# Kernel optimization log

Measured on AMD Instinct MI355X. Metric: run time of the kernel, lower is better.

Reference implementation:

```python
import jax, jax.numpy as jnp
import numpy as np

B, T, DIM, HEADS, MLP_H, R = 64, 197, 768, 12, 3072, 16
HD = DIM // HEADS
EPS = 1e-5
R_EFF = min(R, (T - 1) // 2)  # class token protected


def layernorm(x, g, b):
    m = jnp.mean(x, -1, keepdims=True)
    v = jnp.var(x, -1, keepdims=True)
    return (x - m) * jax.lax.rsqrt(v + EPS) * g + b


def matching_indices(metric):
    # metric: [B, T, HD]; class token (index 0 of 'a' set) protected
    metric = metric / jnp.linalg.norm(metric, axis=-1, keepdims=True)
    a, b = metric[:, ::2], metric[:, 1::2]            # [B,ta,d], [B,tb,d]
    scores = jnp.einsum('bic,bjc->bij', a, b)
    scores = scores.at[:, 0, :].set(-jnp.inf)         # protect cls token
    node_max = jnp.max(scores, axis=-1)
    node_idx = jnp.argmax(scores, axis=-1)
    edge_idx = jnp.argsort(-node_max, axis=-1)        # descending similarity
    unm_idx = edge_idx[:, R_EFF:]
    src_idx = edge_idx[:, :R_EFF]
    dst_idx = jnp.take_along_axis(node_idx, src_idx, axis=-1)
    unm_idx = jnp.sort(unm_idx, axis=1)               # keep cls first (cls token)
    return unm_idx, src_idx, dst_idx


def merge(x, unm_idx, src_idx, dst_idx):
    # x: [B, T, c] -> [B, T - R_EFF, c]; always scatter-add (as in source code)
    src, dst = x[:, ::2], x[:, 1::2]
    unm = jnp.take_along_axis(src, unm_idx[..., None], axis=1)
    sel = jnp.take_along_axis(src, src_idx[..., None], axis=1)
    bidx = jnp.arange(x.shape[0])[:, None]
    dst = dst.at[bidx, dst_idx].add(sel)
    return jnp.concatenate([unm, dst], axis=1)


def block(x, attn_size, ln1_g, ln1_b, w_qkv, w_proj, b_proj,
          ln2_g, ln2_b, w_fc1, b_fc1, w_fc2, b_fc2):
    # --- attention with log-size bias ---
    h = layernorm(x, ln1_g, ln1_b)
    qkv = (h @ w_qkv.T).reshape(B, T, 3, HEADS, HD).transpose(2, 0, 3, 1, 4)
    q, k, v = qkv[0], qkv[1], qkv[2]                  # [B,H,T,HD]
    attn = jnp.einsum('bhid,bhjd->bhij', q, k) * (HD ** -0.5)
    attn = attn + jnp.log(attn_size)[:, None, None, :, 0]
    attn = jax.nn.softmax(attn, axis=-1)
    o = jnp.einsum('bhij,bhjd->bhid', attn, v).transpose(0, 2, 1, 3).reshape(B, T, DIM)
    x = x + (o @ w_proj.T + b_proj)
    metric = jax.lax.stop_gradient(jnp.mean(k, axis=1))  # [B,T,HD]; no_grad in torch
    # --- ToMe bipartite soft matching ---
    unm_idx, src_idx, dst_idx = matching_indices(metric)
    # source tracking (adjacency initial tokens -> merged groups)
    source = jnp.broadcast_to(jnp.eye(T, dtype=x.dtype), (B, T, T))
    source = merge(source, unm_idx, src_idx, dst_idx)     # [B, Tn, T]
    tn = source.shape[1]
    rci = jnp.max(source * jnp.arange(1, tn + 1, dtype=x.dtype)[:, None], axis=-2)
    rci = (rci - 2.0)[:, 1:]                              # cls_token branch
    # size-weighted average merge
    xs = merge(x * attn_size, unm_idx, src_idx, dst_idx)
    new_size = merge(attn_size, unm_idx, src_idx, dst_idx)
    x = xs / new_size
    # --- MLP ---
    h2 = layernorm(x, ln2_g, ln2_b)
    h2 = jax.nn.gelu(h2 @ w_fc1.T + b_fc1, approximate=False)
    x = x + (h2 @ w_fc2.T + b_fc2)
    return x, new_size, rci


def setup_inputs() -> dict:
    key = jax.random.key(0)
    ks = jax.random.split(key, 6)
    return dict(
        x=jax.random.normal(ks[0], (B, T, DIM), jnp.float32),
        attn_size=jnp.ones((B, T, 1), jnp.float32),
        ln1_g=jnp.ones((DIM,), jnp.float32),
        ln1_b=jnp.zeros((DIM,), jnp.float32),
        w_qkv=jax.random.normal(ks[1], (3 * DIM, DIM), jnp.float32) * 0.02,
        w_proj=jax.random.normal(ks[2], (DIM, DIM), jnp.float32) * 0.02,
        b_proj=jnp.zeros((DIM,), jnp.float32),
        ln2_g=jnp.ones((DIM,), jnp.float32),
        ln2_b=jnp.zeros((DIM,), jnp.float32),
        w_fc1=jax.random.normal(ks[3], (MLP_H, DIM), jnp.float32) * 0.02,
        b_fc1=jnp.zeros((MLP_H,), jnp.float32),
        w_fc2=jax.random.normal(ks[4], (DIM, MLP_H), jnp.float32) * 0.02,
        b_fc2=jnp.zeros((DIM,), jnp.float32),
    )


def reference(x, attn_size, ln1_g, ln1_b, w_qkv, w_proj, b_proj,
              ln2_g, ln2_b, w_fc1, b_fc1, w_fc2, b_fc2):
    return block(x, attn_size, ln1_g, ln1_b, w_qkv, w_proj, b_proj,
                 ln2_g, ln2_b, w_fc1, b_fc1, w_fc2, b_fc2)
```

## Files before the change

### kernel.cpp

```cpp
#include <hip/hip_runtime.h>
#include <cstdint>
#include <cstddef>

#define DEVFN __device__ __forceinline__

typedef __attribute__((ext_vector_type(8))) short short8;
typedef __attribute__((ext_vector_type(4))) float f32x4;
typedef __attribute__((ext_vector_type(2))) long long2v;

#define GLOAD_LDS16(gaddr, laddr)                                              \
  __builtin_amdgcn_global_load_lds(                                            \
      (const __attribute__((address_space(1))) uint32_t*)(gaddr),              \
      (__attribute__((address_space(3))) uint32_t*)(laddr), 16, 0, 0)

constexpr int B_ = 64, T_ = 197, DIM_ = 768, H_ = 12, HD_ = 64, MLP_ = 3072;
constexpr int N_ = B_ * T_;
constexpr int NE_ = 99, NO_ = 98, REFF_ = 16;
constexpr int TM_ = (NE_ - REFF_) + NO_;
constexpr int NM_ = B_ * TM_;

constexpr size_t BOFF_A    = 0;
constexpr size_t BOFF_GBC  = 0;
constexpr size_t BOFF_B    = 58097664;
constexpr size_t BOFF_C    = 77463552;
constexpr size_t BOFF_D    = 113049600;
constexpr size_t BOFF_WKM  = 130842624;
constexpr size_t BOFF_RT   = 131039232;
constexpr size_t BOFF_NSZ  = 131873280;
constexpr size_t BOFF_WQB  = 131919616;
constexpr size_t BOFF_WPB  = 135458560;
constexpr size_t BOFF_W1B  = 136638208;
constexpr size_t BOFF_W2B  = 141356800;

DEVFN ushort f2b(float f) {
  union { float f; uint u; } c; c.f = f;
  uint u = c.u;
  u = (u + 0x7FFFu + ((u >> 16) & 1u)) >> 16;
  return (ushort)u;
}
DEVFN float b2f(ushort h) {
  union { uint u; float f; } c; c.u = ((uint)h) << 16;
  return c.f;
}
DEVFN uchar f2e4m3(float v) {
  return (uchar)__builtin_amdgcn_cvt_pk_fp8_f32(v, 0.f, 0, false);
}
DEVFN uint pk4_fp8(float a, float b, float c, float d) {
  int r = __builtin_amdgcn_cvt_pk_fp8_f32(a, b, 0, false);
  r = __builtin_amdgcn_cvt_pk_fp8_f32(c, d, r, true);
  return (uint)r;
}

DEVFN float fast_gelu(float x) {
  float x3 = x * x * x;
  float z2 = 2.0f * 0.7978845608028654f * fmaf(0.044715f, x3, x);
  z2 = fminf(fmaxf(z2, -60.0f), 60.0f);
  float e = __expf(z2);
  float th = (e - 1.0f) / (e + 1.0f);
  return 0.5f * x * (1.0f + th);
}

DEVFN float wave_sum(float v) {
#pragma unroll
  for (int o = 32; o; o >>= 1) v += __shfl_down(v, o, 64);
  return v;
}
DEVFN float block_sum(float v, float* red) {
  v = wave_sum(v);
  int lane = threadIdx.x & 63, wid = threadIdx.x >> 6;
  __syncthreads();
  if (lane == 0) red[wid] = v;
  __syncthreads();
  return red[0] + red[1] + red[2] + red[3];
}

constexpr int SEG0 = 3 * DIM_ * DIM_;
constexpr int SEG1 = SEG0 + DIM_ * DIM_;
constexpr int SEG2 = SEG1 + MLP_ * DIM_;
constexpr int SEG3 = SEG2 + DIM_ * MLP_;
__global__ __launch_bounds__(256) void f2ball_kernel(
    const float* __restrict__ s0, const float* __restrict__ s1,
    const float* __restrict__ s2, const float* __restrict__ s3,
    uchar* __restrict__ d0, ushort* __restrict__ d1,
    uchar* __restrict__ d2, uchar* __restrict__ d3) {
  int i = (blockIdx.x * 256 + threadIdx.x) * 4;
  if (i >= SEG3) return;
  if (i >= SEG0 && i < SEG1) {
    int off = i - SEG0;
    float4 v = *reinterpret_cast<const float4*>(s1 + off);
    ushort4 o;
    o.x = f2b(v.x); o.y = f2b(v.y); o.z = f2b(v.z); o.w = f2b(v.w);
    *reinterpret_cast<ushort4*>(d1 + off) = o;
  } else {
    const float* src; uchar* dst; int off;
    if (i < SEG0)      { src = s0; dst = d0; off = i; }
    else if (i < SEG2) { src = s2; dst = d2; off = i - SEG1; }
    else               { src = s3; dst = d3; off = i - SEG2; }
    float4 v = *reinterpret_cast<const float4*>(src + off);
    *reinterpret_cast<uint*>(dst + off) = pk4_fp8(v.x, v.y, v.z, v.w);
  }
}

__global__ __launch_bounds__(256) void ln_kernel(
    const float* __restrict__ x, const float* __restrict__ g,
    const float* __restrict__ bb, float* __restrict__ outf,
    uchar* __restrict__ out8) {
  __shared__ float red[4];
  size_t row = blockIdx.x;
  const float* xr = x + row * DIM_;
  int tid = threadIdx.x;
  float s = 0.f;
  for (int i = tid; i < DIM_; i += 256) s += xr[i];
  s = block_sum(s, red);
  float mean = s * (1.0f / DIM_);
  float vs = 0.f;
  for (int i = tid; i < DIM_; i += 256) { float d = xr[i] - mean; vs = fmaf(d, d, vs); }
  vs = block_sum(vs, red);
  float rstd = rsqrtf(vs * (1.0f / DIM_) + 1e-5f);
  for (int i = tid; i < DIM_; i += 256) {
    float v = (xr[i] - mean) * rstd * g[i] + bb[i];
    if (outf) outf[row * DIM_ + i] = v;
    out8[row * DIM_ + i] = f2e4m3(v);
  }
}

__global__ __launch_bounds__(256) void wkmean_kernel(const float* __restrict__ wqkv,
                                                     float* __restrict__ wkm) {
  int idx = blockIdx.x * 256 + threadIdx.x;
  if (idx >= HD_ * DIM_) return;
  int d = idx / DIM_, c = idx % DIM_;
  float s = 0.f;
  for (int h2 = 0; h2 < H_; h2++) s += wqkv[(size_t)(DIM_ + h2 * HD_ + d) * DIM_ + c];
  wkm[idx] = s * (1.0f / H_);
}

__global__ __launch_bounds__(256) void gemm_bt(
    const float* __restrict__ A, const float* __restrict__ Bm,
    float* __restrict__ C, int M, int Nn, int K) {
  __shared__ float As[16][65];
  __shared__ float Bs[16][65];
  const int tid = threadIdx.x;
  const int tx = tid & 15, ty = tid >> 4;
  const int m0 = blockIdx.y * 64, n0 = blockIdx.x * 64;
  float acc[4][4] = {};
  for (int k0 = 0; k0 < K; k0 += 16) {
#pragma unroll
    for (int l = 0; l < 4; ++l) {
      int idx = tid + l * 256;
      int mm = idx >> 4, kk = idx & 15;
      As[kk][mm] = A[(size_t)(m0 + mm) * K + (k0 + kk)];
      Bs[kk][mm] = Bm[(size_t)(n0 + mm) * K + (k0 + kk)];
    }
    __syncthreads();
#pragma unroll
    for (int kk = 0; kk < 16; ++kk) {
      float av[4], bv[4];
#pragma unroll
      for (int i = 0; i < 4; i++) av[i] = As[kk][ty * 4 + i];
#pragma unroll
      for (int j = 0; j < 4; j++) bv[j] = Bs[kk][tx * 4 + j];
#pragma unroll
      for (int i = 0; i < 4; i++)
#pragma unroll
        for (int j = 0; j < 4; j++) acc[i][j] = fmaf(av[i], bv[j], acc[i][j]);
    }
    __syncthreads();
  }
#pragma unroll
  for (int i = 0; i < 4; i++) {
    size_t base = (size_t)(m0 + ty * 4 + i) * Nn + n0 + tx * 4;
#pragma unroll
    for (int j = 0; j < 4; j++) C[base + j] = acc[i][j];
  }
}

__global__ __launch_bounds__(256) void gemm_mfma(
    const ushort* __restrict__ A, const ushort* __restrict__ Bw,
    const float* __restrict__ bias, const float* __restrict__ res,
    float* __restrict__ Cf, ushort* __restrict__ Cb,
    int M, int Nn, int K, int act) {
  __shared__ ushort As[3][128][32];
  __shared__ ushort Bs[3][128][32];
  const int t = threadIdx.x;
  const int wid = t >> 6, l = t & 63;
  const int wrow = wid >> 1, wcol = wid & 1;
  const int lr = l & 15, lk = l >> 4;
  const int lrow = l >> 2, lseg = l & 3;
  const int sswz = lseg ^ ((lrow >> 1) & 3);
  const int rswz = (lr >> 1) & 3;

  const int nwg = (int)gridDim.x;
  const int gx = Nn >> 7;
  const int bid = (int)blockIdx.x;
  const int q = nwg >> 3, r = nwg & 7;
  const int xcd = bid & 7, sub = bid >> 3;
  const int wgid = (xcd < r ? xcd * (q + 1) : r * (q + 1) + (xcd - r) * q) + sub;
  const int m0 = (wgid / gx) * 128, n0 = (wgid % gx) * 128;

  int rA0 = m0 + wid * 32 + lrow;      rA0 = rA0 < M ? rA0 : M - 1;
  int rA1 = m0 + wid * 32 + 16 + lrow; rA1 = rA1 < M ? rA1 : M - 1;
  const ushort* gA0 = A + (size_t)rA0 * K + sswz * 8;
  const ushort* gA1 = A + (size_t)rA1 * K + sswz * 8;
  const ushort* gB0 = Bw + (size_t)(n0 + wid * 32 + lrow) * K + sswz * 8;
  const ushort* gB1 = Bw + (size_t)(n0 + wid * 32 + 16 + lrow) * K + sswz * 8;

  f32x4 acc[4][4];
#pragma unroll
  for (int i = 0; i < 4; i++)
#pragma unroll
    for (int j = 0; j < 4; j++) acc[i][j] = (f32x4){0.f, 0.f, 0.f, 0.f};

  auto STAGE = [&](int buf, int kt) {
    const int k0 = kt * 32;
    GLOAD_LDS16(gA0 + k0, &As[buf][wid * 32][0]);
    GLOAD_LDS16(gB0 + k0, &Bs[buf][wid * 32][0]);
    GLOAD_LDS16(gA1 + k0, &As[buf][wid * 32 + 16][0]);
    GLOAD_LDS16(gB1 + k0, &Bs[buf][wid * 32 + 16][0]);
  };

  const int NT = K >> 5;
  STAGE(0, 0);
  STAGE(1, 1);
  asm volatile("s_waitcnt vmcnt(4)" ::: "memory");
  __builtin_amdgcn_s_barrier();

  for (int kt = 0; kt < NT; kt++) {
    const bool ahead = (kt + 2 < NT);
    if (ahead) STAGE((kt + 2) % 3, kt + 2);
    const int cur = kt % 3;
    short8 af[4], bf[4];
#pragma unroll
    for (int mi = 0; mi < 4; mi++)
      af[mi] = *reinterpret_cast<const short8*>(
          &As[cur][wrow * 64 + mi * 16 + lr][(lk ^ rswz) * 8]);
#pragma unroll
    for (int nj = 0; nj < 4; nj++)
      bf[nj] = *reinterpret_cast<const short8*>(
          &Bs[cur][wcol * 64 + nj * 16 + lr][(lk ^ rswz) * 8]);
#pragma unroll
    for (int mi = 0; mi < 4; mi++)
#pragma unroll
      for (int nj = 0; nj < 4; nj++)
        acc[mi][nj] = __builtin_amdgcn_mfma_f32_16x16x32_bf16(af[mi], bf[nj], acc[mi][nj], 0, 0, 0);
    if (ahead) asm volatile("s_waitcnt vmcnt(4)" ::: "memory");
    else       asm volatile("s_waitcnt vmcnt(0)" ::: "memory");
    __builtin_amdgcn_s_barrier();
  }

#pragma unroll
  for (int mi = 0; mi < 4; mi++) {
    int rbase = m0 + wrow * 64 + mi * 16 + lk * 4;
#pragma unroll
    for (int nj = 0; nj < 4; nj++) {
      int col = n0 + wcol * 64 + nj * 16 + lr;
      float bv = bias ? bias[col] : 0.f;
#pragma unroll
      for (int j = 0; j < 4; j++) {
        int row = rbase + j;
        if (row >= M) continue;
        float v = acc[mi][nj][j] + bv;
        if (act) v = fast_gelu(v);
        size_t idx = (size_t)row * Nn + col;
        if (res) v += res[idx];
        if (Cf) Cf[idx] = v;
        else Cb[idx] = f2b(v);
      }
    }
  }
}

__global__ __launch_bounds__(512) void gemm_fp8_w(
    const uchar* __restrict__ A, const uchar* __restrict__ Bw,
    const float* __restrict__ bias, ushort* __restrict__ Cb,
    uchar* __restrict__ C8, int M, int Nn, int K, int act) {
  __shared__ uchar As[3][128][64];
  __shared__ uchar Bs[3][256][64];
  const int t = threadIdx.x;
  const int wid = t >> 6, l = t & 63;
  const int wm = wid >> 2, wn = wid & 3;
  const int lr = l & 15, lk = l >> 4;
  const int l4 = l >> 2, lseg = l & 3;
  const int sswz = lseg ^ ((l4 >> 1) & 3);
  const int roff = (lk ^ ((lr >> 1) & 3)) * 16;

  const int nwg = (int)gridDim.x;
  const int gx = Nn >> 8;
  const int bid = (int)blockIdx.x;
  const int q = nwg >> 3, r = nwg & 7;
  const int xcd = bid & 7, sub = bid >> 3;
  const int wgid = (xcd < r ? xcd * (q + 1) : r * (q + 1) + (xcd - r) * q) + sub;
  const int m0 = (wgid / gx) * 128, n0 = (wgid % gx) * 256;

  int rA = m0 + wid * 16 + l4; rA = rA < M ? rA : M - 1;
  const uchar* gA0 = A + (size_t)rA * K + sswz * 16;
  const uchar* gB0 = Bw + (size_t)(n0 + wid * 32 + l4) * K + sswz * 16;
  const uchar* gB1 = Bw + (size_t)(n0 + wid * 32 + 16 + l4) * K + sswz * 16;

  f32x4 acc[4][4];
#pragma unroll
  for (int i = 0; i < 4; i++)
#pragma unroll
    for (int j = 0; j < 4; j++) acc[i][j] = (f32x4){0.f, 0.f, 0.f, 0.f};

  auto STAGE = [&](int buf, int kt) {
    const int k0 = kt * 64;
    GLOAD_LDS16(gA0 + k0, &As[buf][wid * 16][0]);
    GLOAD_LDS16(gB0 + k0, &Bs[buf][wid * 32][0]);
    GLOAD_LDS16(gB1 + k0, &Bs[buf][wid * 32 + 16][0]);
  };

  const int NT = K >> 6;
  STAGE(0, 0);
  STAGE(1, 1);
  asm volatile("s_waitcnt vmcnt(3)" ::: "memory");
  __builtin_amdgcn_s_barrier();

  for (int kt = 0; kt < NT; kt++) {
    const bool ahead = (kt + 2 < NT);
    if (ahead) STAGE((kt + 2) % 3, kt + 2);
    const int cur = kt % 3;
    long2v av[4], bv[4];
#pragma unroll
    for (int mi = 0; mi < 4; mi++)
      av[mi] = *reinterpret_cast<const long2v*>(&As[cur][wm * 64 + mi * 16 + lr][roff]);
#pragma unroll
    for (int nj = 0; nj < 4; nj++)
      bv[nj] = *reinterpret_cast<const long2v*>(&Bs[cur][wn * 64 + nj * 16 + lr][roff]);
#pragma unroll
    for (int mi = 0; mi < 4; mi++)
#pragma unroll
      for (int nj = 0; nj < 4; nj++)
        acc[mi][nj] = __builtin_amdgcn_mfma_f32_16x16x32_fp8_fp8(
            av[mi].x, bv[nj].x, acc[mi][nj], 0, 0, 0);
#pragma unroll
    for (int mi = 0; mi < 4; mi++)
#pragma unroll
      for (int nj = 0; nj < 4; nj++)
        acc[mi][nj] = __builtin_amdgcn_mfma_f32_16x16x32_fp8_fp8(
            av[mi].y, bv[nj].y, acc[mi][nj], 0, 0, 0);
    if (ahead) asm volatile("s_waitcnt vmcnt(3)" ::: "memory");
    else       asm volatile("s_waitcnt vmcnt(0)" ::: "memory");
    __builtin_amdgcn_s_barrier();
  }

#pragma unroll
  for (int mi = 0; mi < 4; mi++) {
    int rbase = m0 + wm * 64 + mi * 16 + lk * 4;
#pragma unroll
    for (int nj = 0; nj < 4; nj++) {
      int col = n0 + wn * 64 + nj * 16 + lr;
      float bvv = bias ? bias[col] : 0.f;
#pragma unroll
      for (int j = 0; j < 4; j++) {
        int row = rbase + j;
        if (row >= M) continue;
        float v = acc[mi][nj][j] + bvv;
        if (act) v = fast_gelu(v);
        size_t idx = (size_t)row * Nn + col;
        if (Cb) Cb[idx] = f2b(v);
        else C8[idx] = f2e4m3(v);
      }
    }
  }
}

__global__ __launch_bounds__(256) void gemm_fp8(
    const uchar* __restrict__ A, const uchar* __restrict__ Bw,
    const float* __restrict__ bias, const float* __restrict__ res,
    float* __restrict__ Cf, int M, int Nn, int K) {
  __shared__ uchar As[3][128][64];
  __shared__ uchar Bs[3][128][64];
  const int t = threadIdx.x;
  const int wid = t >> 6, l = t & 63;
  const int wrow = wid >> 1, wcol = wid & 1;
  const int lr = l & 15, lk = l >> 4;
  const int l4 = l >> 2, lseg = l & 3;
  const int sswz = lseg ^ ((l4 >> 1) & 3);
  const int roff = (lk ^ ((lr >> 1) & 3)) * 16;

  const int nwg = (int)gridDim.x;
  const int gx = Nn >> 7;
  const int bid = (int)blockIdx.x;
  const int q = nwg >> 3, r = nwg & 7;
  const int xcd = bid & 7, sub = bid >> 3;
  const int wgid = (xcd < r ? xcd * (q + 1) : r * (q + 1) + (xcd - r) * q) + sub;
  const int m0 = (wgid / gx) * 128, n0 = (wgid % gx) * 128;

  int rA0 = m0 + wid * 32 + l4;      rA0 = rA0 < M ? rA0 : M - 1;
  int rA1 = m0 + wid * 32 + 16 + l4; rA1 = rA1 < M ? rA1 : M - 1;
  const uchar* gA0 = A + (size_t)rA0 * K + sswz * 16;
  const uchar* gA1 = A + (size_t)rA1 * K + sswz * 16;
  const uchar* gB0 = Bw + (size_t)(n0 + wid * 32 + l4) * K + sswz * 16;
  const uchar* gB1 = Bw + (size_t)(n0 + wid * 32 + 16 + l4) * K + sswz * 16;

  f32x4 acc[4][4];
#pragma unroll
  for (int i = 0; i < 4; i++)
#pragma unroll
    for (int j = 0; j < 4; j++) acc[i][j] = (f32x4){0.f, 0.f, 0.f, 0.f};

  auto STAGE = [&](int buf, int kt) {
    const int k0 = kt * 64;
    GLOAD_LDS16(gA0 + k0, &As[buf][wid * 32][0]);
    GLOAD_LDS16(gB0 + k0, &Bs[buf][wid * 32][0]);
    GLOAD_LDS16(gA1 + k0, &As[buf][wid * 32 + 16][0]);
    GLOAD_LDS16(gB1 + k0, &Bs[buf][wid * 32 + 16][0]);
  };

  const int NT = K >> 6;
  STAGE(0, 0);
  STAGE(1, 1);
  asm volatile("s_waitcnt vmcnt(4)" ::: "memory");
  __builtin_amdgcn_s_barrier();

  for (int kt = 0; kt < NT; kt++) {
    const bool ahead = (kt + 2 < NT);
    if (ahead) STAGE((kt + 2) % 3, kt + 2);
    const int cur = kt % 3;
    long2v av[4], bv[4];
#pragma unroll
    for (int mi = 0; mi < 4; mi++)
      av[mi] = *reinterpret_cast<const long2v*>(&As[cur][wrow * 64 + mi * 16 + lr][roff]);
#pragma unroll
    for (int nj = 0; nj < 4; nj++)
      bv[nj] = *reinterpret_cast<const long2v*>(&Bs[cur][wcol * 64 + nj * 16 + lr][roff]);
#pragma unroll
    for (int mi = 0; mi < 4; mi++)
#pragma unroll
      for (int nj = 0; nj < 4; nj++)
        acc[mi][nj] = __builtin_amdgcn_mfma_f32_16x16x32_fp8_fp8(
            av[mi].x, bv[nj].x, acc[mi][nj], 0, 0, 0);
#pragma unroll
    for (int mi = 0; mi < 4; mi++)
#pragma unroll
      for (int nj = 0; nj < 4; nj++)
        acc[mi][nj] = __builtin_amdgcn_mfma_f32_16x16x32_fp8_fp8(
            av[mi].y, bv[nj].y, acc[mi][nj], 0, 0, 0);
    if (ahead) asm volatile("s_waitcnt vmcnt(4)" ::: "memory");
    else       asm volatile("s_waitcnt vmcnt(0)" ::: "memory");
    __builtin_amdgcn_s_barrier();
  }

#pragma unroll
  for (int mi = 0; mi < 4; mi++) {
    int rbase = m0 + wrow * 64 + mi * 16 + lk * 4;
#pragma unroll
    for (int nj = 0; nj < 4; nj++) {
      int col = n0 + wcol * 64 + nj * 16 + lr;
      float bvv = bias[col];
#pragma unroll
      for (int j = 0; j < 4; j++) {
        int row = rbase + j;
        if (row >= M) continue;
        size_t idx = (size_t)row * Nn + col;
        Cf[idx] = acc[mi][nj][j] + bvv + res[idx];
      }
    }
  }
}

__global__ __launch_bounds__(512) void attn3_kernel(
    const ushort* __restrict__ qkv, const float* __restrict__ asize,
    ushort* __restrict__ o) {
  __shared__ ushort Kb[208][72];
  __shared__ ushort Vt[64][232];
  __shared__ ushort Plds[8][16][232];
  __shared__ float lb[200];
  const int bh = blockIdx.x;
  const int h = bh % H_, b = bh / H_;
  const size_t bT = (size_t)b * T_;
  const int tid = threadIdx.x;
  const int l = tid & 63, wid = tid >> 6;
  const int lr = l & 15, lk = l >> 4;

  for (int j = tid; j < T_; j += 512) lb[j] = logf(asize[bT + j]);
  for (int idx = tid; idx < 208 * 8; idx += 512) {
    int row = idx >> 3, seg = idx & 7;
    int kr = row < T_ ? row : T_ - 1;
    *reinterpret_cast<uint4*>(&Kb[row][seg * 8]) = *reinterpret_cast<const uint4*>(
        qkv + (bT + kr) * (3 * DIM_) + DIM_ + h * HD_ + seg * 8);
  }
  for (int idx = tid; idx < 197 * 8; idx += 512) {
    int row = idx >> 3, seg = idx & 7;
    uint4 v = *reinterpret_cast<const uint4*>(
        qkv + (bT + row) * (3 * DIM_) + 2 * DIM_ + h * HD_ + seg * 8);
    const ushort* us = reinterpret_cast<const ushort*>(&v);
#pragma unroll
    for (int e = 0; e < 8; e++) Vt[seg * 8 + e][row] = us[e];
  }
  for (int idx = tid; idx < 64 * 35; idx += 512) Vt[idx / 35][197 + idx % 35] = 0;
  for (int i = tid; i < 8 * 16 * 116; i += 512) reinterpret_cast<uint*>(Plds)[i] = 0;
  __syncthreads();

  for (int s = wid; s < 13; s += 8) {
    const int q0 = s * 16;
    int qr = q0 + lr; qr = qr < T_ ? qr : T_ - 1;
    const ushort* qp = qkv + (bT + qr) * (3 * DIM_) + h * HD_;
    short8 aq0 = *reinterpret_cast<const short8*>(qp + lk * 8);
    short8 aq1 = *reinterpret_cast<const short8*>(qp + 32 + lk * 8);

    f32x4 accs[13];
#pragma unroll
    for (int t2 = 0; t2 < 13; t2++) accs[t2] = (f32x4){0.f, 0.f, 0.f, 0.f};
#pragma unroll
    for (int t2 = 0; t2 < 13; t2++) {
      short8 bk0 = *reinterpret_cast<const short8*>(&Kb[t2 * 16 + lr][lk * 8]);
      short8 bk1 = *reinterpret_cast<const short8*>(&Kb[t2 * 16 + lr][32 + lk * 8]);
      accs[t2] = __builtin_amdgcn_mfma_f32_16x16x32_bf16(aq0, bk0, accs[t2], 0, 0, 0);
      accs[t2] = __builtin_amdgcn_mfma_f32_16x16x32_bf16(aq1, bk1, accs[t2], 0, 0, 0);
    }
    const int col0 = lr;
    float m4[4] = {-INFINITY, -INFINITY, -INFINITY, -INFINITY};
#pragma unroll
    for (int t2 = 0; t2 < 13; t2++) {
      int col = t2 * 16 + col0;
      bool valid = col < T_;
      float lbv = valid ? lb[col] : 0.f;
#pragma unroll
      for (int j = 0; j < 4; j++) {
        float v = valid ? fmaf(accs[t2][j], 0.125f, lbv) : -INFINITY;
        accs[t2][j] = v;
        m4[j] = fmaxf(m4[j], v);
      }
    }
#pragma unroll
    for (int off = 1; off < 16; off <<= 1)
#pragma unroll
      for (int j = 0; j < 4; j++) m4[j] = fmaxf(m4[j], __shfl_xor(m4[j], off, 64));
    float s4[4] = {0.f, 0.f, 0.f, 0.f};
#pragma unroll
    for (int t2 = 0; t2 < 13; t2++)
#pragma unroll
      for (int j = 0; j < 4; j++) {
        float e = __expf(accs[t2][j] - m4[j]);
        accs[t2][j] = e;
        s4[j] += e;
      }
#pragma unroll
    for (int off = 1; off < 16; off <<= 1)
#pragma unroll
      for (int j = 0; j < 4; j++) s4[j] += __shfl_xor(s4[j], off, 64);
    float inv4[4];
#pragma unroll
    for (int j = 0; j < 4; j++) inv4[j] = 1.0f / s4[j];
#pragma unroll
    for (int t2 = 0; t2 < 13; t2++)
#pragma unroll
      for (int j = 0; j < 4; j++)
        Plds[wid][lk * 4 + j][t2 * 16 + col0] = f2b(accs[t2][j] * inv4[j]);

    f32x4 acco[4];
#pragma unroll
    for (int ct = 0; ct < 4; ct++) acco[ct] = (f32x4){0.f, 0.f, 0.f, 0.f};
#pragma unroll
    for (int kt = 0; kt < 7; kt++) {
      short8 ap = *reinterpret_cast<const short8*>(&Plds[wid][lr][kt * 32 + lk * 8]);
#pragma unroll
      for (int ct = 0; ct < 4; ct++) {
        short8 bv = *reinterpret_cast<const short8*>(&Vt[ct * 16 + lr][kt * 32 + lk * 8]);
        acco[ct] = __builtin_amdgcn_mfma_f32_16x16x32_bf16(ap, bv, acco[ct], 0, 0, 0);
      }
    }
#pragma unroll
    for (int ct = 0; ct < 4; ct++)
#pragma unroll
      for (int j = 0; j < 4; j++) {
        int row = q0 + lk * 4 + j;
        if (row < T_)
          o[(bT + row) * DIM_ + h * HD_ + ct * 16 + lr] = f2b(acco[ct][j]);
      }
  }
}

__global__ __launch_bounds__(256) void match_kernel(
    const float* __restrict__ metric, const float* __restrict__ asize,
    int* __restrict__ route, float* __restrict__ nsz,
    float* __restrict__ out_ns, float* __restrict__ out_rci) {
  __shared__ float m[197][65];
  __shared__ float nmax[99];
  __shared__ int nidx[99];
  __shared__ int rnk[99];
  __shared__ int srcr[16];
  __shared__ int dstr[16];
  __shared__ int unmp[99];
  int b = blockIdx.x;
  int tid = threadIdx.x;
  int lane = tid & 63, wid = tid >> 6;

  if (tid < T_) {
    const float* mr = metric + ((size_t)b * T_ + tid) * HD_;
    float ss = 0.f;
#pragma unroll
    for (int d = 0; d < 64; d++) { float v = mr[d]; ss = fmaf(v, v, ss); }
    float nrm = sqrtf(ss);
#pragma unroll
    for (int d = 0; d < 64; d++) m[tid][d] = mr[d] / nrm;
  }
  __syncthreads();

  for (int i = wid; i < NE_; i += 4) {
    if (i == 0) {
      if (lane == 0) { nmax[0] = -INFINITY; nidx[0] = 0; }
      continue;
    }
    float bv = -INFINITY;
    int bj = 1 << 30;
    for (int j = lane; j < NO_; j += 64) {
      const float* a = m[2 * i];
      const float* bb = m[2 * j + 1];
      float sdot = 0.f;
#pragma unroll
      for (int d = 0; d < 64; d++) sdot = fmaf(a[d], bb[d], sdot);
      if (sdot > bv) { bv = sdot; bj = j; }
    }
#pragma unroll
    for (int off = 32; off; off >>= 1) {
      float ov = __shfl_down(bv, off, 64);
      int oj = __shfl_down(bj, off, 64);
      if (ov > bv || (ov == bv && oj < bj)) { bv = ov; bj = oj; }
    }
    if (lane == 0) { nmax[i] = bv; nidx[i] = bj; }
  }
  __syncthreads();

  if (tid < NE_) {
    float v = nmax[tid];
    int r = 0;
    for (int i2 = 0; i2 < NE_; i2++) {
      float v2 = nmax[i2];
      r += (v2 > v) || (v2 == v && i2 < tid);
    }
    rnk[tid] = r;
  }
  __syncthreads();
  if (tid < NE_ && rnk[tid] < REFF_) { srcr[rnk[tid]] = tid; dstr[rnk[tid]] = nidx[tid]; }
  __syncthreads();
  if (tid < NE_ && rnk[tid] >= REFF_) {
    int p = 0;
    for (int i2 = 0; i2 < tid; i2++) p += (rnk[i2] >= REFF_);
    unmp[tid] = p;
    int* rr = route + ((size_t)b * TM_ + p) * 18;
    rr[0] = 1;
    rr[1] = 2 * tid;
  }
  if (tid < NO_) {
    int d = tid;
    int* rr = route + ((size_t)b * TM_ + (NE_ - REFF_) + d) * 18;
    int cnt = 1;
    rr[1] = 2 * d + 1;
    for (int r = 0; r < REFF_; r++)
      if (dstr[r] == d) { cnt++; rr[cnt] = 2 * srcr[r]; }
    rr[0] = cnt;
  }
  __syncthreads();

  for (int row = tid; row < TM_; row += 256) {
    const int* rr = route + ((size_t)b * TM_ + row) * 18;
    int cnt = rr[0];
    float s = 0.f;
    for (int t2 = 0; t2 < cnt; t2++) s += asize[(size_t)b * T_ + rr[1 + t2]];
    out_ns[(size_t)b * TM_ + row] = s;
    nsz[(size_t)b * TM_ + row] = s;
  }
  for (int t = 1 + tid; t < T_; t += 256) {
    int val;
    if (t & 1) {
      val = (NE_ - REFF_ - 1) + ((t - 1) >> 1);
    } else {
      int i = t >> 1;
      val = (rnk[i] >= REFF_) ? (unmp[i] - 1) : ((NE_ - REFF_ - 1) + nidx[i]);
    }
    out_rci[(size_t)b * (T_ - 1) + (t - 1)] = (float)val;
  }
}

__global__ __launch_bounds__(256) void merge_ln_kernel(
    const float* __restrict__ x1, const float* __restrict__ asize,
    const int* __restrict__ route, const float* __restrict__ nsz,
    const float* __restrict__ g, const float* __restrict__ bb,
    float* __restrict__ xm, uchar* __restrict__ h28) {
  int row = blockIdx.x;
  int b = row / TM_;
  const int* rr = route + (size_t)row * 18;
  __shared__ int cnt_s;
  __shared__ int toks[17];
  __shared__ float szs[17];
  __shared__ float red[4];
  int tid = threadIdx.x;
  if (tid == 0) cnt_s = rr[0];
  __syncthreads();
  int cnt = cnt_s;
  if (tid < cnt) {
    int t = rr[1 + tid];
    toks[tid] = t;
    szs[tid] = asize[(size_t)b * T_ + t];
  }
  __syncthreads();
  float ns = nsz[row];
  float val[3];
#pragma unroll
  for (int p = 0; p < 3; p++) {
    int e = tid + p * 256;
    float acc = 0.f;
    for (int c2 = 0; c2 < cnt; c2++)
      acc = fmaf(x1[((size_t)b * T_ + toks[c2]) * DIM_ + e], szs[c2], acc);
    val[p] = acc / ns;
    xm[(size_t)row * DIM_ + e] = val[p];
  }
  float s = val[0] + val[1] + val[2];
  s = block_sum(s, red);
  float mean = s * (1.0f / DIM_);
  float vs = 0.f;
#pragma unroll
  for (int p = 0; p < 3; p++) { float d = val[p] - mean; vs = fmaf(d, d, vs); }
  vs = block_sum(vs, red);
  float rstd = rsqrtf(vs * (1.0f / DIM_) + 1e-5f);
#pragma unroll
  for (int p = 0; p < 3; p++) {
    int e = tid + p * 256;
    h28[(size_t)row * DIM_ + e] = f2e4m3((val[p] - mean) * rstd * g[e] + bb[e]);
  }
}

extern "C" void kernel_launch(void* const* d_in, const int* in_sizes, int n_in,
                              void* d_out, int out_size, void* d_ws, size_t ws_size,
                              hipStream_t stream) {
  const float* x_in = (const float*)d_in[0];
  const float* asize = (const float*)d_in[1];
  const float* ln1g = (const float*)d_in[2];
  const float* ln1b = (const float*)d_in[3];
  const float* wqkv = (const float*)d_in[4];
  const float* wproj = (const float*)d_in[5];
  const float* bproj = (const float*)d_in[6];
  const float* ln2g = (const float*)d_in[7];
  const float* ln2b = (const float*)d_in[8];
  const float* wfc1 = (const float*)d_in[9];
  const float* bfc1 = (const float*)d_in[10];
  const float* wfc2 = (const float*)d_in[11];
  const float* bfc2 = (const float*)d_in[12];

  char* base = (char*)d_ws;
  float* h    = (float*)(base + BOFF_A);
  ushort* qkvb = (ushort*)(base + BOFF_A);
  float* x1   = (float*)(base + BOFF_A);
  uchar* gbc8 = (uchar*)(base + BOFF_GBC);
  uchar* h8   = (uchar*)(base + BOFF_B);
  ushort* ob  = (ushort*)(base + BOFF_B);
  float* xm   = (float*)(base + BOFF_C);
  float* met  = (float*)(base + BOFF_D);
  uchar* h28  = (uchar*)(base + BOFF_D);
  float* wkm  = (float*)(base + BOFF_WKM);
  int* route  = (int*)(base + BOFF_RT);
  float* nsz  = (float*)(base + BOFF_NSZ);
  uchar* w8q  = (uchar*)(base + BOFF_WQB);
  ushort* wpb = (ushort*)(base + BOFF_WPB);
  uchar* w18  = (uchar*)(base + BOFF_W1B);
  uchar* w28  = (uchar*)(base + BOFF_W2B);

  float* out_x = (float*)d_out;
  float* out_ns = out_x + (size_t)NM_ * DIM_;
  float* out_rci = out_ns + NM_;

  f2ball_kernel<<<(SEG3 / 4 + 255) / 256, 256, 0, stream>>>(
      wqkv, wproj, wfc1, wfc2, w8q, wpb, w18, w28);
  wkmean_kernel<<<(HD_ * DIM_ + 255) / 256, 256, 0, stream>>>(wqkv, wkm);

  ln_kernel<<<N_, 256, 0, stream>>>(x_in, ln1g, ln1b, h, h8);
  gemm_bt<<<dim3(1, N_ / 64), 256, 0, stream>>>(h, wkm, met, N_, HD_, DIM_);
  gemm_fp8_w<<<((N_ + 127) / 128) * (3 * DIM_ / 256), 512, 0, stream>>>(
      h8, w8q, nullptr, qkvb, nullptr, N_, 3 * DIM_, DIM_, 0);
  attn3_kernel<<<B_ * H_, 512, 0, stream>>>(qkvb, asize, ob);
  gemm_mfma<<<(DIM_ / 128) * ((N_ + 127) / 128), 256, 0, stream>>>(
      ob, wpb, bproj, x_in, x1, nullptr, N_, DIM_, DIM_, 0);
  match_kernel<<<B_, 256, 0, stream>>>(met, asize, route, nsz, out_ns, out_rci);
  merge_ln_kernel<<<NM_, 256, 0, stream>>>(x1, asize, route, nsz, ln2g, ln2b, xm, h28);

  gemm_fp8_w<<<((NM_ + 127) / 128) * (MLP_ / 256), 512, 0, stream>>>(
      h28, w18, bfc1, nullptr, gbc8, NM_, MLP_, DIM_, 1);
  gemm_fp8<<<(DIM_ / 128) * ((NM_ + 127) / 128), 256, 0, stream>>>(
      gbc8, w28, bfc2, xm, out_x, NM_, DIM_, MLP_);
}
```

Baseline: 502.6 us.

## Switch attention PV and output projection to FP8 with swizzled LDS layout

Runs the attention P·V product in FP8 MFMA. P and V are stored as e4m3 in XOR-swizzled LDS tiles, and the attention output is written as FP8. The output projection now uses the existing FP8 GEMM with FP8-converted proj weights instead of the bf16 MFMA GEMM, which is deleted. This halves operand bytes and raises MFMA throughput for these stages, at the cost of lower precision in softmax probabilities, V and the attention output.

```diff
diff --git a/kernel.cpp b/kernel.cpp
--- a/kernel.cpp
+++ b/kernel.cpp
@@ -22,6 +22,7 @@
 constexpr size_t BOFF_A    = 0;
 constexpr size_t BOFF_GBC  = 0;
 constexpr size_t BOFF_B    = 58097664;
+constexpr size_t BOFF_O8   = 67780608;
 constexpr size_t BOFF_C    = 77463552;
 constexpr size_t BOFF_D    = 113049600;
 constexpr size_t BOFF_WKM  = 130842624;
@@ -81,24 +82,17 @@
 __global__ __launch_bounds__(256) void f2ball_kernel(
     const float* __restrict__ s0, const float* __restrict__ s1,
     const float* __restrict__ s2, const float* __restrict__ s3,
-    uchar* __restrict__ d0, ushort* __restrict__ d1,
+    uchar* __restrict__ d0, uchar* __restrict__ d1,
     uchar* __restrict__ d2, uchar* __restrict__ d3) {
   int i = (blockIdx.x * 256 + threadIdx.x) * 4;
   if (i >= SEG3) return;
-  if (i >= SEG0 && i < SEG1) {
-    int off = i - SEG0;
-    float4 v = *reinterpret_cast<const float4*>(s1 + off);
-    ushort4 o;
-    o.x = f2b(v.x); o.y = f2b(v.y); o.z = f2b(v.z); o.w = f2b(v.w);
-    *reinterpret_cast<ushort4*>(d1 + off) = o;
-  } else {
-    const float* src; uchar* dst; int off;
-    if (i < SEG0)      { src = s0; dst = d0; off = i; }
-    else if (i < SEG2) { src = s2; dst = d2; off = i - SEG1; }
-    else               { src = s3; dst = d3; off = i - SEG2; }
-    float4 v = *reinterpret_cast<const float4*>(src + off);
-    *reinterpret_cast<uint*>(dst + off) = pk4_fp8(v.x, v.y, v.z, v.w);
-  }
+  const float* src; uchar* dst; int off;
+  if (i < SEG0)      { src = s0; dst = d0; off = i; }
+  else if (i < SEG1) { src = s1; dst = d1; off = i - SEG0; }
+  else if (i < SEG2) { src = s2; dst = d2; off = i - SEG1; }
+  else               { src = s3; dst = d3; off = i - SEG2; }
+  float4 v = *reinterpret_cast<const float4*>(src + off);
+  *reinterpret_cast<uint*>(dst + off) = pk4_fp8(v.x, v.y, v.z, v.w);
 }
 
 __global__ __launch_bounds__(256) void ln_kernel(
@@ -174,101 +168,6 @@
   }
 }
 
-__global__ __launch_bounds__(256) void gemm_mfma(
-    const ushort* __restrict__ A, const ushort* __restrict__ Bw,
-    const float* __restrict__ bias, const float* __restrict__ res,
-    float* __restrict__ Cf, ushort* __restrict__ Cb,
-    int M, int Nn, int K, int act) {
-  __shared__ ushort As[3][128][32];
-  __shared__ ushort Bs[3][128][32];
-  const int t = threadIdx.x;
-  const int wid = t >> 6, l = t & 63;
-  const int wrow = wid >> 1, wcol = wid & 1;
-  const int lr = l & 15, lk = l >> 4;
-  const int lrow = l >> 2, lseg = l & 3;
-  const int sswz = lseg ^ ((lrow >> 1) & 3);
-  const int rswz = (lr >> 1) & 3;
-
-  const int nwg = (int)gridDim.x;
-  const int gx = Nn >> 7;
-  const int bid = (int)blockIdx.x;
-  const int q = nwg >> 3, r = nwg & 7;
-  const int xcd = bid & 7, sub = bid >> 3;
-  const int wgid = (xcd < r ? xcd * (q + 1) : r * (q + 1) + (xcd - r) * q) + sub;
-  const int m0 = (wgid / gx) * 128, n0 = (wgid % gx) * 128;
-
-  int rA0 = m0 + wid * 32 + lrow;      rA0 = rA0 < M ? rA0 : M - 1;
-  int rA1 = m0 + wid * 32 + 16 + lrow; rA1 = rA1 < M ? rA1 : M - 1;
-  const ushort* gA0 = A + (size_t)rA0 * K + sswz * 8;
-  const ushort* gA1 = A + (size_t)rA1 * K + sswz * 8;
-  const ushort* gB0 = Bw + (size_t)(n0 + wid * 32 + lrow) * K + sswz * 8;
-  const ushort* gB1 = Bw + (size_t)(n0 + wid * 32 + 16 + lrow) * K + sswz * 8;
-
-  f32x4 acc[4][4];
-#pragma unroll
-  for (int i = 0; i < 4; i++)
-#pragma unroll
-    for (int j = 0; j < 4; j++) acc[i][j] = (f32x4){0.f, 0.f, 0.f, 0.f};
-
-  auto STAGE = [&](int buf, int kt) {
-    const int k0 = kt * 32;
-    GLOAD_LDS16(gA0 + k0, &As[buf][wid * 32][0]);
-    GLOAD_LDS16(gB0 + k0, &Bs[buf][wid * 32][0]);
-    GLOAD_LDS16(gA1 + k0, &As[buf][wid * 32 + 16][0]);
-    GLOAD_LDS16(gB1 + k0, &Bs[buf][wid * 32 + 16][0]);
-  };
-
-  const int NT = K >> 5;
-  STAGE(0, 0);
-  STAGE(1, 1);
-  asm volatile("s_waitcnt vmcnt(4)" ::: "memory");
-  __builtin_amdgcn_s_barrier();
-
-  for (int kt = 0; kt < NT; kt++) {
-    const bool ahead = (kt + 2 < NT);
-    if (ahead) STAGE((kt + 2) % 3, kt + 2);
-    const int cur = kt % 3;
-    short8 af[4], bf[4];
-#pragma unroll
-    for (int mi = 0; mi < 4; mi++)
-      af[mi] = *reinterpret_cast<const short8*>(
-          &As[cur][wrow * 64 + mi * 16 + lr][(lk ^ rswz) * 8]);
-#pragma unroll
-    for (int nj = 0; nj < 4; nj++)
-      bf[nj] = *reinterpret_cast<const short8*>(
-          &Bs[cur][wcol * 64 + nj * 16 + lr][(lk ^ rswz) * 8]);
-#pragma unroll
-    for (int mi = 0; mi < 4; mi++)
-#pragma unroll
-      for (int nj = 0; nj < 4; nj++)
-        acc[mi][nj] = __builtin_amdgcn_mfma_f32_16x16x32_bf16(af[mi], bf[nj], acc[mi][nj], 0, 0, 0);
-    if (ahead) asm volatile("s_waitcnt vmcnt(4)" ::: "memory");
-    else       asm volatile("s_waitcnt vmcnt(0)" ::: "memory");
-    __builtin_amdgcn_s_barrier();
-  }
-
-#pragma unroll
-  for (int mi = 0; mi < 4; mi++) {
-    int rbase = m0 + wrow * 64 + mi * 16 + lk * 4;
-#pragma unroll
-    for (int nj = 0; nj < 4; nj++) {
-      int col = n0 + wcol * 64 + nj * 16 + lr;
-      float bv = bias ? bias[col] : 0.f;
-#pragma unroll
-      for (int j = 0; j < 4; j++) {
-        int row = rbase + j;
-        if (row >= M) continue;
-        float v = acc[mi][nj][j] + bv;
-        if (act) v = fast_gelu(v);
-        size_t idx = (size_t)row * Nn + col;
-        if (res) v += res[idx];
-        if (Cf) Cf[idx] = v;
-        else Cb[idx] = f2b(v);
-      }
-    }
-  }
-}
-
 __global__ __launch_bounds__(512) void gemm_fp8_w(
     const uchar* __restrict__ A, const uchar* __restrict__ Bw,
     const float* __restrict__ bias, ushort* __restrict__ Cb,
@@ -459,12 +358,12 @@
   }
 }
 
-__global__ __launch_bounds__(512) void attn3_kernel(
+__global__ __launch_bounds__(512) void attn4_kernel(
     const ushort* __restrict__ qkv, const float* __restrict__ asize,
-    ushort* __restrict__ o) {
+    uchar* __restrict__ o8) {
   __shared__ ushort Kb[208][72];
-  __shared__ ushort Vt[64][232];
-  __shared__ ushort Plds[8][16][232];
+  __shared__ uchar Vt8[64][256];
+  __shared__ uchar P8[8][16][256];
   __shared__ float lb[200];
   const int bh = blockIdx.x;
   const int h = bh % H_, b = bh / H_;
@@ -473,6 +372,10 @@
   const int l = tid & 63, wid = tid >> 6;
   const int lr = l & 15, lk = l >> 4;
 
+  for (int i = tid; i < 4096; i += 512) reinterpret_cast<uint*>(Vt8)[i] = 0;
+  for (int i = tid; i < 8192; i += 512) reinterpret_cast<uint*>(P8)[i] = 0;
+  __syncthreads();
+
   for (int j = tid; j < T_; j += 512) lb[j] = logf(asize[bT + j]);
   for (int idx = tid; idx < 208 * 8; idx += 512) {
     int row = idx >> 3, seg = idx & 7;
@@ -481,15 +384,17 @@
         qkv + (bT + kr) * (3 * DIM_) + DIM_ + h * HD_ + seg * 8);
   }
   for (int idx = tid; idx < 197 * 8; idx += 512) {
-    int row = idx >> 3, seg = idx & 7;
+    int k = idx >> 3, seg = idx & 7;
     uint4 v = *reinterpret_cast<const uint4*>(
-        qkv + (bT + row) * (3 * DIM_) + 2 * DIM_ + h * HD_ + seg * 8);
+        qkv + (bT + k) * (3 * DIM_) + 2 * DIM_ + h * HD_ + seg * 8);
     const ushort* us = reinterpret_cast<const ushort*>(&v);
-#pragma unroll
-    for (int e = 0; e < 8; e++) Vt[seg * 8 + e][row] = us[e];
-  }
-  for (int idx = tid; idx < 64 * 35; idx += 512) Vt[idx / 35][197 + idx % 35] = 0;
-  for (int i = tid; i < 8 * 16 * 116; i += 512) reinterpret_cast<uint*>(Plds)[i] = 0;
+    const int slot = k >> 4, kin = k & 15;
+#pragma unroll
+    for (int e = 0; e < 8; e++) {
+      int d = seg * 8 + e;
+      Vt8[d][((slot ^ (d & 7)) << 4) + kin] = f2e4m3(b2f(us[e]));
+    }
+  }
   __syncthreads();
 
   for (int s = wid; s < 13; s += 8) {
@@ -546,19 +451,23 @@
 #pragma unroll
     for (int t2 = 0; t2 < 13; t2++)
 #pragma unroll
-      for (int j = 0; j < 4; j++)
-        Plds[wid][lk * 4 + j][t2 * 16 + col0] = f2b(accs[t2][j] * inv4[j]);
+      for (int j = 0; j < 4; j++) {
+        int rr = lk * 4 + j;
+        P8[wid][rr][((t2 ^ (rr & 7)) << 4) + col0] = f2e4m3(accs[t2][j] * inv4[j]);
+      }
 
     f32x4 acco[4];
 #pragma unroll
     for (int ct = 0; ct < 4; ct++) acco[ct] = (f32x4){0.f, 0.f, 0.f, 0.f};
 #pragma unroll
-    for (int kt = 0; kt < 7; kt++) {
-      short8 ap = *reinterpret_cast<const short8*>(&Plds[wid][lr][kt * 32 + lk * 8]);
+    for (int i = 0; i < 4; i++) {
+      const int po = ((i * 4 + lk) ^ (lr & 7)) * 16;
+      long2v pa = *reinterpret_cast<const long2v*>(&P8[wid][lr][po]);
 #pragma unroll
       for (int ct = 0; ct < 4; ct++) {
-        short8 bv = *reinterpret_cast<const short8*>(&Vt[ct * 16 + lr][kt * 32 + lk * 8]);
-        acco[ct] = __builtin_amdgcn_mfma_f32_16x16x32_bf16(ap, bv, acco[ct], 0, 0, 0);
+        long2v vb = *reinterpret_cast<const long2v*>(&Vt8[ct * 16 + lr][po]);
+        acco[ct] = __builtin_amdgcn_mfma_f32_16x16x32_fp8_fp8(pa.x, vb.x, acco[ct], 0, 0, 0);
+        acco[ct] = __builtin_amdgcn_mfma_f32_16x16x32_fp8_fp8(pa.y, vb.y, acco[ct], 0, 0, 0);
       }
     }
 #pragma unroll
@@ -567,7 +476,7 @@
       for (int j = 0; j < 4; j++) {
         int row = q0 + lk * 4 + j;
         if (row < T_)
-          o[(bT + row) * DIM_ + h * HD_ + ct * 16 + lr] = f2b(acco[ct][j]);
+          o8[(bT + row) * DIM_ + h * HD_ + ct * 16 + lr] = f2e4m3(acco[ct][j]);
       }
   }
 }
@@ -745,7 +654,7 @@
   float* x1   = (float*)(base + BOFF_A);
   uchar* gbc8 = (uchar*)(base + BOFF_GBC);
   uchar* h8   = (uchar*)(base + BOFF_B);
-  ushort* ob  = (ushort*)(base + BOFF_B);
+  uchar* o8   = (uchar*)(base + BOFF_O8);
   float* xm   = (float*)(base + BOFF_C);
   float* met  = (float*)(base + BOFF_D);
   uchar* h28  = (uchar*)(base + BOFF_D);
@@ -753,7 +662,7 @@
   int* route  = (int*)(base + BOFF_RT);
   float* nsz  = (float*)(base + BOFF_NSZ);
   uchar* w8q  = (uchar*)(base + BOFF_WQB);
-  ushort* wpb = (ushort*)(base + BOFF_WPB);
+  uchar* w8p  = (uchar*)(base + BOFF_WPB);
   uchar* w18  = (uchar*)(base + BOFF_W1B);
   uchar* w28  = (uchar*)(base + BOFF_W2B);
 
@@ -762,16 +671,16 @@
   float* out_rci = out_ns + NM_;
 
   f2ball_kernel<<<(SEG3 / 4 + 255) / 256, 256, 0, stream>>>(
-      wqkv, wproj, wfc1, wfc2, w8q, wpb, w18, w28);
+      wqkv, wproj, wfc1, wfc2, w8q, w8p, w18, w28);
   wkmean_kernel<<<(HD_ * DIM_ + 255) / 256, 256, 0, stream>>>(wqkv, wkm);
 
   ln_kernel<<<N_, 256, 0, stream>>>(x_in, ln1g, ln1b, h, h8);
   gemm_bt<<<dim3(1, N_ / 64), 256, 0, stream>>>(h, wkm, met, N_, HD_, DIM_);
   gemm_fp8_w<<<((N_ + 127) / 128) * (3 * DIM_ / 256), 512, 0, stream>>>(
       h8, w8q, nullptr, qkvb, nullptr, N_, 3 * DIM_, DIM_, 0);
-  attn3_kernel<<<B_ * H_, 512, 0, stream>>>(qkvb, asize, ob);
-  gemm_mfma<<<(DIM_ / 128) * ((N_ + 127) / 128), 256, 0, stream>>>(
-      ob, wpb, bproj, x_in, x1, nullptr, N_, DIM_, DIM_, 0);
+  attn4_kernel<<<B_ * H_, 512, 0, stream>>>(qkvb, asize, o8);
+  gemm_fp8<<<(DIM_ / 128) * ((N_ + 127) / 128), 256, 0, stream>>>(
+      o8, w8p, bproj, x_in, x1, N_, DIM_, DIM_);
   match_kernel<<<B_, 256, 0, stream>>>(met, asize, route, nsz, out_ns, out_rci);
   merge_ln_kernel<<<NM_, 256, 0, stream>>>(x1, asize, route, nsz, ln2g, ln2b, xm, h28);
 
```

Measured after the change: 475.9 us. -5.3%, faster.
